# Optimization experiments

Measured on AMD Instinct MI355X. Metric: run time of the kernel, lower is better.

Reference implementation:

```python
import jax, jax.numpy as jnp
import numpy as np

B, T, C = 64, 256, 384
H = 6
D = C // H  # head_size = 64


def setup_inputs() -> dict:
    key = jax.random.key(0)
    ks = jax.random.split(key, 6)
    s = 1.0 / np.sqrt(C)
    return {
        "x": jax.random.normal(ks[0], (B, T, C), dtype=jnp.float32),
        "Wk": jax.random.uniform(ks[1], (C, C), jnp.float32, -s, s),
        "Wq": jax.random.uniform(ks[2], (C, C), jnp.float32, -s, s),
        "Wv": jax.random.uniform(ks[3], (C, C), jnp.float32, -s, s),
        "Wo": jax.random.uniform(ks[4], (C, C), jnp.float32, -s, s),
        "bo": jax.random.uniform(ks[5], (C,), jnp.float32, -s, s),
    }


def reference(x, Wk, Wq, Wv, Wo, bo):
    b, t, c = x.shape
    # QKV projections (no bias), split heads: [B, H, T, D]
    k = (x @ Wk.T).reshape(b, t, H, D).transpose(0, 2, 1, 3)
    q = (x @ Wq.T).reshape(b, t, H, D).transpose(0, 2, 1, 3)
    v = (x @ Wv.T).reshape(b, t, H, D).transpose(0, 2, 1, 3)
    # Scores scaled by C**-0.5 (as in the original module, not head_size**-0.5)
    wei = jnp.einsum("bhqd,bhkd->bhqk", q, k) * (c ** -0.5)
    mask = jnp.tril(jnp.ones((t, t), dtype=bool))
    wei = jnp.where(mask, wei, -jnp.inf)
    wei = jax.nn.softmax(wei, axis=-1)
    out = jnp.einsum("bhqk,bhkd->bhqd", wei, v)
    out = out.transpose(0, 2, 1, 3).reshape(b, t, c)
    # Output projection (dropout is identity at inference)
    return out @ Wo.T + bo
```

## Files before the change

kernel.cpp:

```cpp
#include <hip/hip_runtime.h>
#include <hip/hip_bf16.h>

typedef unsigned short u16;
typedef __attribute__((ext_vector_type(8))) short short8;
typedef __attribute__((ext_vector_type(4))) float f32x4;

#define BATCH 64
#define SEQ   256
#define CDIM  384
#define NHEAD 6
#define DHEAD 64
#define NROW  16384

constexpr float SCALE = 0.051031036307982884f;

__device__ __forceinline__ f32x4 mfma16(short8 a, short8 b, f32x4 c) {
    return __builtin_amdgcn_mfma_f32_16x16x32_bf16(a, b, c, 0, 0, 0);
}

__device__ __forceinline__ u16 f2b(float f) {
    __hip_bfloat16 h = __float2bfloat16(f);
    return *reinterpret_cast<u16*>(&h);
}

__device__ __forceinline__ short8 pack8(const float* __restrict__ p) {
    const float4 a = *(const float4*)p;
    const float4 b = *(const float4*)(p + 4);
    short8 r;
    r[0] = (short)f2b(a.x); r[1] = (short)f2b(a.y);
    r[2] = (short)f2b(a.z); r[3] = (short)f2b(a.w);
    r[4] = (short)f2b(b.x); r[5] = (short)f2b(b.y);
    r[6] = (short)f2b(b.z); r[7] = (short)f2b(b.w);
    return r;
}

__global__ __launch_bounds__(256) void gemm_qkv(
        const float* __restrict__ X, const float* __restrict__ Wk,
        const float* __restrict__ Wv, const float* __restrict__ Wq,
        u16* __restrict__ Kd, u16* __restrict__ VTd, u16* __restrict__ Qd)
{
    __shared__ u16 SMEM[17408];
    u16* As = SMEM;
    u16* Bs = SMEM + 4096;

    const int n0 = blockIdx.x * 128;
    const int m0 = blockIdx.y * 128;
    const int z  = blockIdx.z;
    const float* W = (z == 0) ? Wk : (z == 1 ? Wv : Wq);

    const int tid  = threadIdx.x;
    const int lane = tid & 63;
    const int wv   = tid >> 6;
    const int l15  = lane & 15;
    const int q4   = lane >> 4;
    const int wm   = (wv >> 1) * 64;
    const int wn   = (wv & 1) * 64;

    f32x4 acc[4][4] = {};

    for (int kk = 0; kk < CDIM; kk += 32) {
        short8 areg[2], breg[2];
#pragma unroll
        for (int ch = 0; ch < 2; ++ch) {
            const int f = (ch * 256 + tid) * 8;
            const int r = f >> 5;
            const int c = f & 31;
            areg[ch] = pack8(X + (size_t)(m0 + r) * CDIM + kk + c);
            breg[ch] = pack8(W + (size_t)(n0 + r) * CDIM + kk + c);
        }
        __syncthreads();
#pragma unroll
        for (int ch = 0; ch < 2; ++ch) {
            const int f = (ch * 256 + tid) * 8;
            *(short8*)(As + f) = areg[ch];
            *(short8*)(Bs + f) = breg[ch];
        }
        __syncthreads();

        short8 af[4], bf[4];
#pragma unroll
        for (int t = 0; t < 4; ++t) {
            af[t] = *(const short8*)(As + (wm + t * 16 + l15) * 32 + q4 * 8);
            bf[t] = *(const short8*)(Bs + (wn + t * 16 + l15) * 32 + q4 * 8);
        }
#pragma unroll
        for (int tm = 0; tm < 4; ++tm)
#pragma unroll
            for (int tn = 0; tn < 4; ++tn)
                acc[tm][tn] = mfma16(af[tm], bf[tn], acc[tm][tn]);
    }

    if (z != 1) {
        u16* D = (z == 0) ? Kd : Qd;
#pragma unroll
        for (int tm = 0; tm < 4; ++tm)
#pragma unroll
            for (int tn = 0; tn < 4; ++tn) {
                const int col = n0 + wn + tn * 16 + l15;
#pragma unroll
                for (int r = 0; r < 4; ++r) {
                    const int row = m0 + wm + tm * 16 + q4 * 4 + r;
                    const int b = row >> 8, t = row & 255;
                    const int h = col >> 6, d = col & 63;
                    D[(size_t)((b * NHEAD + h) * SEQ + t) * DHEAD + d] =
                        f2b(acc[tm][tn][r]);
                }
            }
    } else {
        __syncthreads();
        u16* T = SMEM;
#pragma unroll
        for (int tm = 0; tm < 4; ++tm)
#pragma unroll
            for (int tn = 0; tn < 4; ++tn) {
                const int cl = wn + tn * 16 + l15;
#pragma unroll
                for (int r = 0; r < 4; ++r) {
                    const int rl = wm + tm * 16 + q4 * 4 + r;
                    T[cl * 136 + rl] = f2b(acc[tm][tn][r]);
                }
            }
        __syncthreads();
        const int b  = m0 >> 8;
        const int t0 = m0 & 255;
        const int fl = tid >> 1;
        const int hf = tid & 1;
        const int fg = n0 + fl;
        const int h  = fg >> 6, d = fg & 63;
        u16* dst = VTd + ((size_t)(b * NHEAD + h) * DHEAD + d) * SEQ + t0 + hf * 64;
        const u16* src = T + fl * 136 + hf * 64;
#pragma unroll
        for (int j = 0; j < 8; ++j)
            *(uint4*)(dst + j * 8) = *(const uint4*)(src + j * 8);
    }
}

template <int CH>
__device__ __forceinline__ void attn_body(
        const u16* __restrict__ Qg, const u16* __restrict__ Kg,
        const u16* __restrict__ VTg, u16* __restrict__ Og, int bh,
        u16* SA , u16* Pbuf )
{
    constexpr int NKEY = 64 * (CH + 1);
    constexpr int KT   = NKEY / 16;
    constexpr int NPH  = (NKEY + 127) / 128;

    const int tid  = threadIdx.x;
    const int wv   = tid >> 6;
    const int lane = tid & 63;
    const int l15  = lane & 15;
    const int q4   = lane >> 4;
    const int qrow0 = CH * 64 + wv * 16;
    const int qmax  = qrow0 + 15;

    short8 aq[2];
#pragma unroll
    for (int ks = 0; ks < 2; ++ks)
        aq[ks] = *(const short8*)(Qg + (size_t)(bh * SEQ + qrow0 + l15) * DHEAD
                                     + ks * 32 + q4 * 8);

    u16* Kbuf = SA;
    f32x4 s[KT];
#pragma unroll
    for (int ph = 0; ph < NPH; ++ph) {
        const int rows = (NKEY - ph * 128) < 128 ? (NKEY - ph * 128) : 128;
        for (int it = 0; it < rows / 32; ++it) {
            const int r  = it * 32 + (tid >> 3);
            const int d0 = (tid & 7) * 8;
            *(uint4*)(Kbuf + r * 72 + d0) =
                *(const uint4*)(Kg + (size_t)(bh * SEQ + ph * 128 + r) * DHEAD + d0);
        }
        __syncthreads();
#pragma unroll
        for (int t = 0; t < rows / 16; ++t) {
            const int gt = ph * 8 + t;
            if (gt * 16 <= qmax) {
                f32x4 z = {0.f, 0.f, 0.f, 0.f};
#pragma unroll
                for (int ks = 0; ks < 2; ++ks) {
                    short8 bk = *(const short8*)(Kbuf + (t * 16 + l15) * 72
                                                 + ks * 32 + q4 * 8);
                    z = mfma16(aq[ks], bk, z);
                }
                const int kc = gt * 16 + l15;
#pragma unroll
                for (int r = 0; r < 4; ++r) {
                    float v = z[r] * SCALE;
                    if (kc > qrow0 + q4 * 4 + r) v = -1e30f;
                    z[r] = v;
                }
                s[gt] = z;
            } else {
                f32x4 neg = {-1e30f, -1e30f, -1e30f, -1e30f};
                s[gt] = neg;
            }
        }
        __syncthreads();
    }

    float mx[4], sm[4], rs[4];
#pragma unroll
    for (int r = 0; r < 4; ++r) {
        float m = -1e30f;
#pragma unroll
        for (int t = 0; t < KT; ++t) m = fmaxf(m, s[t][r]);
#pragma unroll
        for (int off = 1; off < 16; off <<= 1)
            m = fmaxf(m, __shfl_xor(m, off, 16));
        mx[r] = m;
        sm[r] = 0.f;
    }
#pragma unroll
    for (int t = 0; t < KT; ++t)
#pragma unroll
        for (int r = 0; r < 4; ++r) {
            float p = __expf(s[t][r] - mx[r]);
            s[t][r] = p;
            sm[r] += p;
        }
#pragma unroll
    for (int r = 0; r < 4; ++r) {
#pragma unroll
        for (int off = 1; off < 16; off <<= 1)
            sm[r] += __shfl_xor(sm[r], off, 16);
        rs[r] = 1.f / sm[r];
    }

    u16* Vt = SA;
    u16* Pw = Pbuf + wv * 16 * 40;
    f32x4 o[4] = {};
#pragma unroll
    for (int ph = 0; ph < NPH; ++ph) {
        const int rows = (NKEY - ph * 128) < 128 ? (NKEY - ph * 128) : 128;
        const int cpr  = rows >> 3;
#pragma unroll
        for (int it = 0; it < 4; ++it) {
            if (it < cpr / 4) {
                const int flat = it * 256 + tid;
                const int rd = flat / cpr;
                const int kc = (flat - rd * cpr) * 8;
                *(uint4*)(Vt + rd * 136 + kc) =
                    *(const uint4*)(VTg + ((size_t)bh * DHEAD + rd) * SEQ
                                        + ph * 128 + kc);
            }
        }
        __syncthreads();
#pragma unroll
        for (int ks = 0; ks < rows / 32; ++ks) {
            const int gks = ph * 4 + ks;
            if (gks * 32 <= qmax) {
#pragma unroll
                for (int tt = 0; tt < 2; ++tt) {
                    const int gt = gks * 2 + tt;
#pragma unroll
                    for (int r = 0; r < 4; ++r)
                        Pw[(q4 * 4 + r) * 40 + tt * 16 + l15] = f2b(s[gt][r]);
                }
                asm volatile("s_waitcnt lgkmcnt(0)" ::: "memory");
                short8 ap = *(const short8*)(Pw + l15 * 40 + q4 * 8);
#pragma unroll
                for (int tn = 0; tn < 4; ++tn) {
                    short8 bv = *(const short8*)(Vt + (tn * 16 + l15) * 136
                                                 + ks * 32 + q4 * 8);
                    o[tn] = mfma16(ap, bv, o[tn]);
                }
            }
        }
        __syncthreads();
    }

#pragma unroll
    for (int tn = 0; tn < 4; ++tn) {
        const int d = tn * 16 + l15;
#pragma unroll
        for (int r = 0; r < 4; ++r) {
            const int qr = qrow0 + q4 * 4 + r;
            Og[(size_t)(bh * SEQ + qr) * DHEAD + d] = f2b(o[tn][r] * rs[r]);
        }
    }
}

__global__ __launch_bounds__(256) void attn_kernel(
        const u16* __restrict__ Qg, const u16* __restrict__ Kg,
        const u16* __restrict__ VTg, u16* __restrict__ Og)
{
    __shared__ u16 SA[128 * 72];
    __shared__ u16 Pbuf[4 * 16 * 40];
    const int bh = blockIdx.y;
    switch (blockIdx.x) {
        case 0: attn_body<0>(Qg, Kg, VTg, Og, bh, SA, Pbuf); break;
        case 1: attn_body<1>(Qg, Kg, VTg, Og, bh, SA, Pbuf); break;
        case 2: attn_body<2>(Qg, Kg, VTg, Og, bh, SA, Pbuf); break;
        default: attn_body<3>(Qg, Kg, VTg, Og, bh, SA, Pbuf); break;
    }
}

__global__ __launch_bounds__(256) void gemm_out(
        const u16* __restrict__ O, const float* __restrict__ Wo,
        const float* __restrict__ bias, float* __restrict__ out)
{
    __shared__ u16 As[128 * 32];
    __shared__ u16 Bs[128 * 32];

    const int m0 = blockIdx.y * 128;
    const int n0 = blockIdx.x * 128;

    const int tid  = threadIdx.x;
    const int lane = tid & 63;
    const int wv   = tid >> 6;
    const int l15  = lane & 15;
    const int q4   = lane >> 4;
    const int wm   = (wv >> 1) * 64;
    const int wn   = (wv & 1) * 64;

    f32x4 acc[4][4] = {};

    for (int kk = 0; kk < CDIM; kk += 32) {
        uint4 areg[2];
        short8 breg[2];
#pragma unroll
        for (int ch = 0; ch < 2; ++ch) {
            const int f = (ch * 256 + tid) * 8;
            const int r = f >> 5;
            const int c = f & 31;
            const int row = m0 + r;
            const int b = row >> 8, t = row & 255;
            const int k = kk + c;
            const int hh = k >> 6, dd = k & 63;
            areg[ch] = *(const uint4*)(O +
                (size_t)((b * NHEAD + hh) * SEQ + t) * DHEAD + dd);
            breg[ch] = pack8(Wo + (size_t)(n0 + r) * CDIM + kk + c);
        }
        __syncthreads();
#pragma unroll
        for (int ch = 0; ch < 2; ++ch) {
            const int f = (ch * 256 + tid) * 8;
            *(uint4*)(As + f)  = areg[ch];
            *(short8*)(Bs + f) = breg[ch];
        }
        __syncthreads();

        short8 af[4], bf[4];
#pragma unroll
        for (int t = 0; t < 4; ++t) {
            af[t] = *(const short8*)(As + (wm + t * 16 + l15) * 32 + q4 * 8);
            bf[t] = *(const short8*)(Bs + (wn + t * 16 + l15) * 32 + q4 * 8);
        }
#pragma unroll
        for (int tm = 0; tm < 4; ++tm)
#pragma unroll
            for (int tn = 0; tn < 4; ++tn)
                acc[tm][tn] = mfma16(af[tm], bf[tn], acc[tm][tn]);
    }

#pragma unroll
    for (int tm = 0; tm < 4; ++tm) {
#pragma unroll
        for (int tn = 0; tn < 4; ++tn) {
            const int col = n0 + wn + tn * 16 + l15;
            const float bb = bias[col];
#pragma unroll
            for (int r = 0; r < 4; ++r) {
                const int row = m0 + wm + tm * 16 + q4 * 4 + r;
                out[(size_t)row * CDIM + col] = acc[tm][tn][r] + bb;
            }
        }
    }
}

extern "C" void kernel_launch(void* const* d_in, const int* in_sizes, int n_in,
                              void* d_out, int out_size, void* d_ws, size_t ws_size,
                              hipStream_t stream)
{
    const float* x  = (const float*)d_in[0];
    const float* Wk = (const float*)d_in[1];
    const float* Wq = (const float*)d_in[2];
    const float* Wv = (const float*)d_in[3];
    const float* Wo = (const float*)d_in[4];
    const float* bo = (const float*)d_in[5];
    float* out = (float*)d_out;

    const size_t SZ = (size_t)NROW * CDIM;
    u16* Kw  = (u16*)d_ws;
    u16* Qw  = Kw + SZ;
    u16* Ow  = Qw + SZ;
    u16* VTw = (u16*)d_out;

    dim3 g1(CDIM / 128, NROW / 128, 3);
    gemm_qkv<<<g1, 256, 0, stream>>>(x, Wk, Wv, Wq, Kw, VTw, Qw);

    dim3 g2(4, BATCH * NHEAD);
    attn_kernel<<<g2, 256, 0, stream>>>(Qw, Kw, VTw, Ow);

    dim3 g3(CDIM / 128, NROW / 128);
    gemm_out<<<g3, 256, 0, stream>>>(Ow, Wo, bo, out);
}
```

Baseline: 168.8 us.

## Pre-convert inputs to bf16 and stage GEMM tiles via direct global-to-LDS loads

Adds separate conversion kernels that turn x and all four weight matrices into bf16 buffers in the workspace once per call. The QKV and output GEMMs then load bf16 tiles straight into shared memory with global_load_lds, dropping the register staging and the repeated fp32-to-bf16 conversion. The QKV GEMM previously re-read and re-converted x once per output column tile, so reads there shrink. The cost is two extra launches and an extra pass over x: fp32 read plus bf16 write, then a bf16 re-read.

```diff
diff --git a/kernel.cpp b/kernel.cpp
--- a/kernel.cpp
+++ b/kernel.cpp
@@ -23,20 +23,49 @@
     return *reinterpret_cast<u16*>(&h);
 }
 
-__device__ __forceinline__ short8 pack8(const float* __restrict__ p) {
-    const float4 a = *(const float4*)p;
-    const float4 b = *(const float4*)(p + 4);
+__device__ __forceinline__ void gload_lds16(const u16* g, u16* l) {
+    __builtin_amdgcn_global_load_lds(
+        (const __attribute__((address_space(1))) void*)g,
+        (__attribute__((address_space(3))) void*)l, 16, 0, 0);
+}
+
+__global__ __launch_bounds__(256) void cvt_x(
+        const float* __restrict__ s, u16* __restrict__ d)
+{
+    const int i = (blockIdx.x * 256 + threadIdx.x) * 8;
+    const float4 a = *(const float4*)(s + i);
+    const float4 b = *(const float4*)(s + i + 4);
     short8 r;
     r[0] = (short)f2b(a.x); r[1] = (short)f2b(a.y);
     r[2] = (short)f2b(a.z); r[3] = (short)f2b(a.w);
     r[4] = (short)f2b(b.x); r[5] = (short)f2b(b.y);
     r[6] = (short)f2b(b.z); r[7] = (short)f2b(b.w);
-    return r;
+    *(short8*)(d + i) = r;
+}
+
+__global__ __launch_bounds__(256) void cvt_w(
+        const float* __restrict__ w0, const float* __restrict__ w1,
+        const float* __restrict__ w2, const float* __restrict__ w3,
+        u16* __restrict__ d0, u16* __restrict__ d1,
+        u16* __restrict__ d2, u16* __restrict__ d3)
+{
+    const int z = blockIdx.y;
+    const float* s = (z == 0) ? w0 : (z == 1) ? w1 : (z == 2) ? w2 : w3;
+    u16*         d = (z == 0) ? d0 : (z == 1) ? d1 : (z == 2) ? d2 : d3;
+    const int i = (blockIdx.x * 256 + threadIdx.x) * 8;
+    const float4 a = *(const float4*)(s + i);
+    const float4 b = *(const float4*)(s + i + 4);
+    short8 r;
+    r[0] = (short)f2b(a.x); r[1] = (short)f2b(a.y);
+    r[2] = (short)f2b(a.z); r[3] = (short)f2b(a.w);
+    r[4] = (short)f2b(b.x); r[5] = (short)f2b(b.y);
+    r[6] = (short)f2b(b.z); r[7] = (short)f2b(b.w);
+    *(short8*)(d + i) = r;
 }
 
 __global__ __launch_bounds__(256) void gemm_qkv(
-        const float* __restrict__ X, const float* __restrict__ Wk,
-        const float* __restrict__ Wv, const float* __restrict__ Wq,
+        const u16* __restrict__ X, const u16* __restrict__ Wk,
+        const u16* __restrict__ Wv, const u16* __restrict__ Wq,
         u16* __restrict__ Kd, u16* __restrict__ VTd, u16* __restrict__ Qd)
 {
     __shared__ u16 SMEM[17408];
@@ -46,7 +75,7 @@
     const int n0 = blockIdx.x * 128;
     const int m0 = blockIdx.y * 128;
     const int z  = blockIdx.z;
-    const float* W = (z == 0) ? Wk : (z == 1 ? Wv : Wq);
+    const u16* W = (z == 0) ? Wk : (z == 1 ? Wv : Wq);
 
     const int tid  = threadIdx.x;
     const int lane = tid & 63;
@@ -59,21 +88,15 @@
     f32x4 acc[4][4] = {};
 
     for (int kk = 0; kk < CDIM; kk += 32) {
-        short8 areg[2], breg[2];
+        __syncthreads();
 #pragma unroll
         for (int ch = 0; ch < 2; ++ch) {
             const int f = (ch * 256 + tid) * 8;
             const int r = f >> 5;
             const int c = f & 31;
-            areg[ch] = pack8(X + (size_t)(m0 + r) * CDIM + kk + c);
-            breg[ch] = pack8(W + (size_t)(n0 + r) * CDIM + kk + c);
-        }
-        __syncthreads();
-#pragma unroll
-        for (int ch = 0; ch < 2; ++ch) {
-            const int f = (ch * 256 + tid) * 8;
-            *(short8*)(As + f) = areg[ch];
-            *(short8*)(Bs + f) = breg[ch];
+            const int lb = (ch * 256 + wv * 64) * 8;
+            gload_lds16(X + (size_t)(m0 + r) * CDIM + kk + c, As + lb);
+            gload_lds16(W + (size_t)(n0 + r) * CDIM + kk + c, Bs + lb);
         }
         __syncthreads();
 
@@ -139,7 +162,7 @@
 __device__ __forceinline__ void attn_body(
         const u16* __restrict__ Qg, const u16* __restrict__ Kg,
         const u16* __restrict__ VTg, u16* __restrict__ Og, int bh,
-        u16* SA , u16* Pbuf )
+        u16* SA, u16* Pbuf)
 {
     constexpr int NKEY = 64 * (CH + 1);
     constexpr int KT   = NKEY / 16;
@@ -296,14 +319,14 @@
 }
 
 __global__ __launch_bounds__(256) void gemm_out(
-        const u16* __restrict__ O, const float* __restrict__ Wo,
+        const u16* __restrict__ O, const u16* __restrict__ Wo,
         const float* __restrict__ bias, float* __restrict__ out)
 {
     __shared__ u16 As[128 * 32];
     __shared__ u16 Bs[128 * 32];
 
+    const int n0 = blockIdx.x * 128;
     const int m0 = blockIdx.y * 128;
-    const int n0 = blockIdx.x * 128;
 
     const int tid  = threadIdx.x;
     const int lane = tid & 63;
@@ -316,8 +339,7 @@
     f32x4 acc[4][4] = {};
 
     for (int kk = 0; kk < CDIM; kk += 32) {
-        uint4 areg[2];
-        short8 breg[2];
+        __syncthreads();
 #pragma unroll
         for (int ch = 0; ch < 2; ++ch) {
             const int f = (ch * 256 + tid) * 8;
@@ -327,16 +349,10 @@
             const int b = row >> 8, t = row & 255;
             const int k = kk + c;
             const int hh = k >> 6, dd = k & 63;
-            areg[ch] = *(const uint4*)(O +
-                (size_t)((b * NHEAD + hh) * SEQ + t) * DHEAD + dd);
-            breg[ch] = pack8(Wo + (size_t)(n0 + r) * CDIM + kk + c);
-        }
-        __syncthreads();
-#pragma unroll
-        for (int ch = 0; ch < 2; ++ch) {
-            const int f = (ch * 256 + tid) * 8;
-            *(uint4*)(As + f)  = areg[ch];
-            *(short8*)(Bs + f) = breg[ch];
+            const int lb = (ch * 256 + wv * 64) * 8;
+            gload_lds16(O + (size_t)((b * NHEAD + hh) * SEQ + t) * DHEAD + dd,
+                        As + lb);
+            gload_lds16(Wo + (size_t)(n0 + r) * CDIM + kk + c, Bs + lb);
         }
         __syncthreads();
 
@@ -381,17 +397,27 @@
     float* out = (float*)d_out;
 
     const size_t SZ = (size_t)NROW * CDIM;
-    u16* Kw  = (u16*)d_ws;
+    const size_t WZ = (size_t)CDIM * CDIM;
+    u16* xb  = (u16*)d_ws;
+    u16* Wkb = xb  + SZ;
+    u16* Wqb = Wkb + WZ;
+    u16* Wvb = Wqb + WZ;
+    u16* Wob = Wvb + WZ;
+    u16* Kw  = Wob + WZ;
     u16* Qw  = Kw + SZ;
     u16* Ow  = Qw + SZ;
     u16* VTw = (u16*)d_out;
 
+    cvt_x<<<dim3((int)(SZ / 2048)), 256, 0, stream>>>(x, xb);
+    cvt_w<<<dim3((int)(WZ / 2048), 4), 256, 0, stream>>>(
+        Wk, Wq, Wv, Wo, Wkb, Wqb, Wvb, Wob);
+
     dim3 g1(CDIM / 128, NROW / 128, 3);
-    gemm_qkv<<<g1, 256, 0, stream>>>(x, Wk, Wv, Wq, Kw, VTw, Qw);
+    gemm_qkv<<<g1, 256, 0, stream>>>(xb, Wkb, Wvb, Wqb, Kw, VTw, Qw);
 
     dim3 g2(4, BATCH * NHEAD);
     attn_kernel<<<g2, 256, 0, stream>>>(Qw, Kw, VTw, Ow);
 
     dim3 g3(CDIM / 128, NROW / 128);
-    gemm_out<<<g3, 256, 0, stream>>>(Ow, Wo, bo, out);
-}
+    gemm_out<<<g3, 256, 0, stream>>>(Ow, Wob, bo, out);
+}
```

Result: faster. 157.4 us (-6.7%).
